# Optimization experiments

Measured on AMD Instinct MI355X. Metric: run time of the kernel, lower is better.

The kernel has to match this reference:

```python
import jax, jax.numpy as jnp
import numpy as np

B, L, C = 64, 64, 16          # batch, seq_len, chars per word
V, CV = 100000, 100           # word vocab, char vocab
EMB, CHD = 300, 64            # word emb dim, char emb dim
N_HIGHWAY, N_ATTN = 2, 2
D = EMB + 3 * 50              # highway_dim = 450


def setup_inputs() -> dict:
    ks = jax.random.split(jax.random.key(0), 16)
    word_emb = jax.random.normal(ks[6], (V, EMB), jnp.float32) * 0.01
    word_emb = word_emb.at[0].set(0.0)  # padding_idx row zeroed
    return {
        "q1": jax.random.randint(ks[0], (B, L), 0, V),
        "q2": jax.random.randint(ks[1], (B, L), 0, V),
        "q1_len": jax.random.randint(ks[2], (B,), 1, L + 1),
        "q2_len": jax.random.randint(ks[3], (B,), 1, L + 1),
        "q1_char": jax.random.randint(ks[4], (B, L, C), 0, CV),
        "q2_char": jax.random.randint(ks[5], (B, L, C), 0, CV),
        "word_emb": word_emb,
        "char_emb": jax.random.normal(ks[7], (CV, CHD), jnp.float32) * 0.1,
        "conv_w3": jax.random.normal(ks[8], (50, CHD, 3), jnp.float32) / np.sqrt(CHD * 3),
        "conv_b3": jnp.zeros((50,), jnp.float32),
        "conv_w4": jax.random.normal(ks[9], (50, CHD, 4), jnp.float32) / np.sqrt(CHD * 4),
        "conv_b4": jnp.zeros((50,), jnp.float32),
        "conv_w5": jax.random.normal(ks[10], (50, CHD, 5), jnp.float32) / np.sqrt(CHD * 5),
        "conv_b5": jnp.zeros((50,), jnp.float32),
        "hw_w": jax.random.normal(ks[11], (D, D), jnp.float32) / np.sqrt(D),
        "hw_b": jnp.zeros((D,), jnp.float32),
        "attn_w": jax.random.normal(ks[12], (N_ATTN, 3 * D), jnp.float32) / np.sqrt(3 * D),
        "attn_b": jnp.zeros((N_ATTN,), jnp.float32),
    }


def _char_features(qc, emb, convs):
    # qc: [B, T, C] int -> [B, T, 150]
    Bq, T, Cc = qc.shape
    e = emb[qc.reshape(-1, Cc)].transpose(0, 2, 1)  # [B*T, CHD, C]
    outs = []
    for w, b in convs:
        h = jax.lax.conv_general_dilated(e, w, (1,), 'VALID',
                                         dimension_numbers=('NCH', 'OIH', 'NCH'))
        h = jax.nn.relu(h + b[None, :, None])
        outs.append(jnp.max(h, axis=2))  # max over char positions
    return jnp.concatenate(outs, axis=-1).reshape(Bq, T, -1)


def _highway(x, w, b):
    # NB: original reuses the SAME linear for transform and gate (bug-faithful)
    y = x @ w.T + b
    g = jax.nn.sigmoid(y)
    return g * jax.nn.relu(y) + (1.0 - g) * x


def _self_attn(x, mask, w, b):
    # Exact decomposition of Linear(concat(x_i, x_j, x_i*x_j)) -> scalar:
    # score[b,i,j] = x_i.w1 + x_j.w2 + sum_d x_i x_j w3 + b
    d = x.shape[-1]
    w1, w2, w3 = w[:d], w[d:2 * d], w[2 * d:]
    scores = ((x @ w1)[:, :, None] + (x @ w2)[:, None, :]
              + jnp.einsum('bid,bjd->bij', x * w3, x) + b)
    # original masked_fill uses -1e-09 (not -1e9) -- reproduce faithfully
    logits = jnp.where(mask[:, None, :], scores, jnp.float32(-1e-9))
    attn = jax.nn.softmax(logits, axis=-1)
    return jnp.einsum('bij,bjd->bid', attn, x)


def _branch(q, q_char, q_len, word_emb, char_emb, convs, hw_w, hw_b, attn_w, attn_b):
    mask = jnp.arange(L)[None, :] < q_len[:, None]
    x = jnp.concatenate([word_emb[q], _char_features(q_char, char_emb, convs)], axis=-1)
    for _ in range(N_HIGHWAY):
        x = _highway(x, hw_w, hw_b)
    att = x
    for i in range(N_ATTN):
        att = _self_attn(x, mask, attn_w[i], attn_b[i])
        x = att + x
    return att


def reference(q1, q2, q1_len, q2_len, q1_char, q2_char, word_emb, char_emb,
              conv_w3, conv_b3, conv_w4, conv_b4, conv_w5, conv_b5,
              hw_w, hw_b, attn_w, attn_b):
    convs = [(conv_w3, conv_b3), (conv_w4, conv_b4), (conv_w5, conv_b5)]
    a1 = _branch(q1, q1_char, q1_len, word_emb, char_emb, convs, hw_w, hw_b, attn_w, attn_b)
    a2 = _branch(q2, q2_char, q2_len, word_emb, char_emb, convs, hw_w, hw_b, attn_w, attn_b)
    return (a1, a2)
```

## Files before the change

kernel.cpp:

```cpp
#include <hip/hip_runtime.h>
#include <math.h>

#define B   64
#define L   64
#define C   16
#define CHD 64
#define EMB 300
#define D   450
#define DP  480
#define NT  (B*L)
#define NBH 128

typedef short bf16x8 __attribute__((ext_vector_type(8)));
typedef float f32x4  __attribute__((ext_vector_type(4)));
typedef float f32x2  __attribute__((ext_vector_type(2)));
typedef unsigned short ushort_t;
typedef ushort_t us4 __attribute__((ext_vector_type(4)));

#define MFMA16 __builtin_amdgcn_mfma_f32_16x16x32_bf16

#define WPF_N (10 * 10 * 512)
#define WBF_N (32 * 15 * 512)
#define XFRAG 30720

__device__ inline float wave_sum(float v) {
#pragma unroll
    for (int o = 32; o; o >>= 1) v += __shfl_xor(v, o, 64);
    return v;
}
__device__ inline ushort_t f2b(float f) {
    union { float f; unsigned u; } c; c.f = f;
    unsigned r = c.u + 0x7FFFu + ((c.u >> 16) & 1u);
    return (ushort_t)(r >> 16);
}

__global__ __launch_bounds__(256) void prep_kernel(
    const float* __restrict__ W,
    const float* __restrict__ w3, const float* __restrict__ b3,
    const float* __restrict__ w4, const float* __restrict__ b4,
    const float* __restrict__ w5, const float* __restrict__ b5,
    const float* __restrict__ char_emb,
    ushort_t* __restrict__ Wb16F, ushort_t* __restrict__ WpadF,
    float* __restrict__ bias160, ushort_t* __restrict__ ceb16)
{
    int idx = blockIdx.x * 256 + threadIdx.x;
    if (idx < WBF_N) {
        const int e = idx & 7, l = (idx >> 3) & 63, t = idx >> 9;
        const int ks = t % 15, nt = t / 15;
        const int ln = l & 15, q = l >> 4;
        const int n = nt * 16 + ln, k = ks * 32 + q * 8 + e;
        float v = (n < D && k < D) ? W[(size_t)n * D + k] : 0.f;
        Wb16F[idx] = f2b(v);
        return;
    }
    idx -= WBF_N;
    if (idx < WPF_N) {
        const int e = idx & 7, l = (idx >> 3) & 63, t = idx >> 9;
        const int ks = t % 10, nt = t / 10;
        const int ln = l & 15, q = l >> 4;
        const int f = nt * 16 + ln;
        const int kd = ks * 32 + q * 8 + e;
        const int k = kd >> 6, d = kd & 63;
        float v = 0.f;
        if (f < 50)       { if (k < 3) v = w3[f * 192 + d * 3 + k]; }
        else if (f < 100) { if (k < 4) v = w4[(f - 50) * 256 + d * 4 + k]; }
        else if (f < 150) { v = w5[(f - 100) * 320 + d * 5 + k]; }
        WpadF[idx] = f2b(v);
        return;
    }
    idx -= WPF_N;
    if (idx < 160) {
        bias160[idx] = (idx < 50) ? b3[idx] : (idx < 100) ? b4[idx - 50]
                     : (idx < 150) ? b5[idx - 100] : 0.f;
    } else if (idx < 160 + 100 * 64) {
        int i = idx - 160;
        ceb16[i] = f2b(char_emb[i]);
    }
}

#define ESS 72
#define EST (20 * ESS)

__global__ __launch_bounds__(256) void embed_conv_kernel(
    const int* __restrict__ q1, const int* __restrict__ q2,
    const int* __restrict__ q1c, const int* __restrict__ q2c,
    const float* __restrict__ word_emb, const ushort_t* __restrict__ ceb16,
    const ushort_t* __restrict__ WpadF, const float* __restrict__ bias160,
    float* __restrict__ xout, ushort_t* __restrict__ xb16)
{
    __shared__ ushort_t es[8 * EST];

    const int tid  = threadIdx.x;
    const int wv   = tid >> 6;
    const int lane = tid & 63;
    const int ln   = lane & 15, quad = lane >> 4;
    const int bx   = blockIdx.x;
    const int tokbase = ((bx & 7) * 128 + (bx >> 3)) * 8;

#pragma unroll
    for (int i = 0; i < 4; ++i) {
        int c = tid + i * 256;
        int row = c >> 3, part = c & 7;
        int tl = row >> 4, cr = row & 15;
        int gtok   = tokbase + tl;
        int branch = gtok >> 12;
        int tokl   = gtok & (NT - 1);
        int cid    = (branch ? q2c : q1c)[tokl * C + cr];
        *(bf16x8*)&es[tl * EST + cr * ESS + part * 8] =
            *(const bf16x8*)&ceb16[cid * 64 + part * 8];
    }
    {
        int tl = tid >> 5, rr = (tid >> 3) & 3, part = tid & 7;
        bf16x8 z = {0, 0, 0, 0, 0, 0, 0, 0};
        *(bf16x8*)&es[tl * EST + (16 + rr) * ESS + part * 8] = z;
    }

#pragma unroll 1
    for (int c = tid; c < 8 * 75; c += 256) {
        const int t  = c / 75, d4 = c - t * 75;
        const int tok    = tokbase + t;
        const int branch = tok >> 12;
        const int tokl   = tok & (NT - 1);
        const int w      = (branch ? q2 : q1)[tokl];
        const float4 v = *(const float4*)(word_emb + (size_t)w * EMB + d4 * 4);
        float* dst = xout + (size_t)tok * D + d4 * 4;
        *(f32x2*)dst       = (f32x2){v.x, v.y};
        *(f32x2*)(dst + 2) = (f32x2){v.z, v.w};
        us4 pk = { f2b(v.x), f2b(v.y), f2b(v.z), f2b(v.w) };
        *(us4*)(xb16 + (size_t)tok * DP + d4 * 4) = pk;
    }
    if (tid < 240) {
        const int t = tid / 30, k = tid - t * 30;
        xb16[(size_t)(tokbase + t) * DP + D + k] = 0;
    }
    __syncthreads();

    const int t0 = wv * 2, t1 = t0 + 1;
    f32x4 acc[2][10];
#pragma unroll
    for (int t = 0; t < 2; ++t)
#pragma unroll
        for (int nt = 0; nt < 10; ++nt) acc[t][nt] = (f32x4){0.f, 0.f, 0.f, 0.f};

#pragma unroll 1
    for (int ks = 0; ks < 10; ++ks) {
        const int kk   = ks * 32 + quad * 8;
        const int arow = kk >> 6, aoff = kk & 63;
        bf16x8 a0 = *(const bf16x8*)&es[t0 * EST + (ln + arow) * ESS + aoff];
        bf16x8 a1 = *(const bf16x8*)&es[t1 * EST + (ln + arow) * ESS + aoff];
#pragma unroll
        for (int nt = 0; nt < 10; ++nt) {
            bf16x8 bf = *(const bf16x8*)&WpadF[(size_t)((nt * 10 + ks) << 9) + lane * 8];
            acc[0][nt] = MFMA16(a0, bf, acc[0][nt], 0, 0, 0);
            acc[1][nt] = MFMA16(a1, bf, acc[1][nt], 0, 0, 0);
        }
    }
    __syncthreads();

    float* smf = (float*)es;
#pragma unroll
    for (int t = 0; t < 2; ++t) {
        const int tloc = t0 + t;
#pragma unroll
        for (int nt = 0; nt < 10; ++nt) {
            const int f  = nt * 16 + ln;
            const int Pf = (f < 50) ? 14 : (f < 100) ? 13 : 12;
            float m = -1e30f;
#pragma unroll
            for (int r = 0; r < 4; ++r) {
                const int p = quad * 4 + r;
                if (p < Pf) m = fmaxf(m, acc[t][nt][r]);
            }
            m = fmaxf(m, __shfl_xor(m, 16, 64));
            m = fmaxf(m, __shfl_xor(m, 32, 64));
            if (quad == 0) smf[tloc * 160 + f] = fmaxf(0.f, m + bias160[f]);
        }
    }
    __syncthreads();
#pragma unroll 1
    for (int c = tid; c < 8 * 150; c += 256) {
        const int t = c / 150, f = c - t * 150;
        const float rv = smf[t * 160 + f];
        xout[(size_t)(tokbase + t) * D + EMB + f] = rv;
        xb16[(size_t)(tokbase + t) * DP + EMB + f] = f2b(rv);
    }
}

__global__ __launch_bounds__(256, 4) void highway_mfma_kernel(
    const ushort_t* __restrict__ xb16, const float* __restrict__ xf32,
    const ushort_t* __restrict__ Wb16F, const float* __restrict__ bvec,
    float* __restrict__ out, ushort_t* __restrict__ outb16)
{
    const int bx = blockIdx.x;
    const int cx = bx & 7, rr = bx >> 3;
    const int my = cx * 16 + (rr & 15);
    const int mx = rr >> 4;

    const int tid  = threadIdx.x;
    const int wv   = tid >> 6;
    const int lane = tid & 63;
    const int wm = wv >> 1, wn = wv & 1;
    const int m0 = my * 64 + wm * 32;
    const int n0 = mx * 64 + wn * 32;
    const int lm = lane & 15, quad = lane >> 4;

    const ushort_t* ax  = xb16 + (size_t)(m0 + lm) * DP + quad * 8;
    const int ntg0 = mx * 4 + wn * 2;
    const ushort_t* bw0 = Wb16F + (size_t)(ntg0 * 15) * 512 + lane * 8;
    const ushort_t* bw1 = bw0 + 15 * 512;

    f32x4 acc[2][2];
#pragma unroll
    for (int i = 0; i < 2; ++i)
#pragma unroll
        for (int j = 0; j < 2; ++j) acc[i][j] = (f32x4){0.f, 0.f, 0.f, 0.f};

#pragma unroll 3
    for (int ks = 0; ks < 15; ++ks) {
        bf16x8 a0 = *(const bf16x8*)(ax + ks * 32);
        bf16x8 a1 = *(const bf16x8*)(ax + (size_t)16 * DP + ks * 32);
        bf16x8 b0 = *(const bf16x8*)(bw0 + ks * 512);
        bf16x8 b1 = *(const bf16x8*)(bw1 + ks * 512);
        acc[0][0] = MFMA16(a0, b0, acc[0][0], 0, 0, 0);
        acc[0][1] = MFMA16(a0, b1, acc[0][1], 0, 0, 0);
        acc[1][0] = MFMA16(a1, b0, acc[1][0], 0, 0, 0);
        acc[1][1] = MFMA16(a1, b1, acc[1][1], 0, 0, 0);
    }

#pragma unroll
    for (int nt = 0; nt < 2; ++nt) {
        const int n = n0 + nt * 16 + lm;
        const bool nval = (n < D);
        const float bv = nval ? bvec[n] : 0.f;
#pragma unroll
        for (int mt = 0; mt < 2; ++mt) {
#pragma unroll
            for (int r = 0; r < 4; ++r) {
                const int m = m0 + mt * 16 + quad * 4 + r;
                float y = acc[mt][nt][r] + bv;
                float g = 1.f / (1.f + __expf(-y));
                float o = 0.f;
                if (nval) {
                    float xo = xf32[(size_t)m * D + n];
                    o = g * fmaxf(y, 0.f) + (1.f - g) * xo;
                    out[(size_t)m * D + n] = o;
                }
                if (n < DP)
                    outb16[(size_t)m * DP + n] = f2b(nval ? o : 0.f);
            }
        }
    }
}

#define PXS 496

__global__ __launch_bounds__(256) void attn_prep_kernel(
    const float* __restrict__ xf32, const float* __restrict__ attn_w, int layer,
    ushort_t* __restrict__ xF, ushort_t* __restrict__ xw3F, ushort_t* __restrict__ xTF,
    float* __restrict__ s1g, float* __restrict__ s2g)
{
    __shared__ ushort_t Xs[16 * PXS];
    __shared__ ushort_t Xw3s[16 * PXS];

    const int bx  = blockIdx.x;
    const int wid = (bx & 7) * 64 + (bx >> 3);
    const int bh  = wid >> 2, jq = wid & 3;
    const int tid = threadIdx.x;
    const int wv  = tid >> 6;
    const int lane = tid & 63;
    const size_t tok0 = (size_t)bh * 64 + jq * 16;

    const float* wb = attn_w + (size_t)layer * 3 * D;
    const float* w3 = wb + 2 * D;

#pragma unroll 1
    for (int c = tid; c < 16 * 60; c += 256) {
        const int j  = c / 60, k8 = c - j * 60;
        const int k0 = k8 * 8;
        const float* xr = xf32 + (tok0 + j) * D;
        bf16x8 xv, pv;
#pragma unroll
        for (int t = 0; t < 8; ++t) {
            const int k = k0 + t;
            const float x = (k < D) ? xr[k] : 0.f;
            xv[t] = (short)f2b(x);
            pv[t] = (short)f2b((k < D) ? x * w3[k] : 0.f);
        }
        *(bf16x8*)&Xs[j * PXS + k0]   = xv;
        *(bf16x8*)&Xw3s[j * PXS + k0] = pv;
    }

#pragma unroll 1
    for (int rr = 0; rr < 4; ++rr) {
        const int j = wv * 4 + rr;
        const float* xr = xf32 + (tok0 + j) * D;
        float a1 = 0.f, a2 = 0.f;
#pragma unroll
        for (int t = 0; t < 8; ++t) {
            const int k = lane + t * 64;
            if (k < D) {
                float xv = xr[k];
                a1 = fmaf(xv, wb[k], a1);
                a2 = fmaf(xv, wb[D + k], a2);
            }
        }
        a1 = wave_sum(a1);
        a2 = wave_sum(a2);
        if (lane == 0) { s1g[tok0 + j] = a1; s2g[tok0 + j] = a2; }
    }
    __syncthreads();

#pragma unroll 1
    for (int c = tid; c < 960; c += 256) {
        const int ks = c >> 6, l = c & 63;
        const int lnp = l & 15, qp = l >> 4;
        bf16x8 v = *(const bf16x8*)&Xs[lnp * PXS + ks * 32 + qp * 8];
        bf16x8 w = *(const bf16x8*)&Xw3s[lnp * PXS + ks * 32 + qp * 8];
        const size_t o = (size_t)bh * XFRAG + ((jq * 15 + ks) * 64 + l) * 8;
        *(bf16x8*)&xF[o]   = v;
        *(bf16x8*)&xw3F[o] = w;
    }

    {
        const int half = jq >> 1, q0 = (jq & 1) * 2;
#pragma unroll 1
        for (int c = tid; c < 960; c += 256) {
            const int dt = c >> 5, s = c & 31;
            const int qp = q0 + (s >> 4), lnp = s & 15;
            const int d  = dt * 16 + lnp;
            const int jb = (qp & 1) * 8;
            bf16x8 v;
#pragma unroll
            for (int e = 0; e < 8; ++e) v[e] = (short)Xs[(jb + e) * PXS + d];
            *(bf16x8*)&xTF[(size_t)bh * XFRAG + ((dt * 2 + half) * 64 + qp * 16 + lnp) * 8] = v;
        }
    }
}

#define ALS 72

template <bool RES_EMIT>
__global__ __launch_bounds__(256) void attn_fused_kernel(
    const float* __restrict__ xf32,
    const ushort_t* __restrict__ xF, const ushort_t* __restrict__ xw3F,
    const ushort_t* __restrict__ xTF,
    const float* __restrict__ s1g, const float* __restrict__ s2g,
    const int* __restrict__ q1_len, const int* __restrict__ q2_len,
    const float* __restrict__ attn_b, int layer,
    float* __restrict__ outf)
{
    __shared__ float    sc[16][68];
    __shared__ ushort_t Al[16 * ALS];

    const int bx  = blockIdx.x;
    const int wid = (bx & 7) * 64 + (bx >> 3);
    const int bh  = wid >> 2, iq = wid & 3;
    const int branch = bh >> 6, b = bh & 63;
    const int tid  = threadIdx.x;
    const int wv   = tid >> 6;
    const int lane = tid & 63;
    const int ln   = lane & 15, quad = lane >> 4;
    const int i0   = iq * 16;

    const ushort_t* xa = xF   + (size_t)bh * XFRAG + (iq * 15 * 64 + lane) * 8;
    const ushort_t* xb = xw3F + (size_t)bh * XFRAG + (wv * 15 * 64 + lane) * 8;

    f32x4 qa0 = (f32x4){0.f, 0.f, 0.f, 0.f};
    f32x4 qa1 = (f32x4){0.f, 0.f, 0.f, 0.f};
#pragma unroll
    for (int ks = 0; ks < 14; ks += 2) {
        bf16x8 a0 = *(const bf16x8*)(xa + ks * 512);
        bf16x8 b0 = *(const bf16x8*)(xb + ks * 512);
        bf16x8 a1 = *(const bf16x8*)(xa + ks * 512 + 512);
        bf16x8 b1 = *(const bf16x8*)(xb + ks * 512 + 512);
        qa0 = MFMA16(a0, b0, qa0, 0, 0, 0);
        qa1 = MFMA16(a1, b1, qa1, 0, 0, 0);
    }
    {
        bf16x8 a  = *(const bf16x8*)(xa + 14 * 512);
        bf16x8 bq = *(const bf16x8*)(xb + 14 * 512);
        qa0 = MFMA16(a, bq, qa0, 0, 0, 0);
    }
    f32x4 qacc = qa0 + qa1;

    const int   len  = (branch ? q2_len : q1_len)[b];
    const float bias = attn_b[layer];
    const int   j    = wv * 16 + ln;
    const float s2v  = s2g[bh * 64 + j];
#pragma unroll
    for (int reg = 0; reg < 4; ++reg) {
        const int i = i0 + quad * 4 + reg;
        float v = qacc[reg] + s1g[bh * 64 + i] + s2v + bias;
        if (j >= len) v = -1e-9f;
        sc[quad * 4 + reg][j] = v;
    }
    __syncthreads();

#pragma unroll
    for (int rr = 0; rr < 4; ++rr) {
        const int r = wv * 4 + rr;
        float v = sc[r][lane];
        float m = v;
#pragma unroll
        for (int o = 32; o; o >>= 1) m = fmaxf(m, __shfl_xor(m, o, 64));
        float ev = __expf(v - m);
        float sm = ev;
#pragma unroll
        for (int o = 32; o; o >>= 1) sm += __shfl_xor(sm, o, 64);
        Al[r * ALS + lane] = f2b(ev * (1.f / sm));
    }
    __syncthreads();

    const ushort_t* xTb = xTF + (size_t)bh * XFRAG + lane * 8;
    bf16x8 af0 = *(const bf16x8*)&Al[ln * ALS + quad * 8];
    bf16x8 af1 = *(const bf16x8*)&Al[ln * ALS + quad * 8 + 32];

#pragma unroll 2
    for (int dt = wv; dt < 30; dt += 4) {
        bf16x8 b0 = *(const bf16x8*)(xTb + dt * 1024);
        bf16x8 b1 = *(const bf16x8*)(xTb + dt * 1024 + 512);
        f32x4 acc = (f32x4){0.f, 0.f, 0.f, 0.f};
        acc = MFMA16(af0, b0, acc, 0, 0, 0);
        acc = MFMA16(af1, b1, acc, 0, 0, 0);

        const int d = dt * 16 + ln;
        if (d < D) {
#pragma unroll
            for (int reg = 0; reg < 4; ++reg) {
                const int i = i0 + quad * 4 + reg;
                float v = acc[reg];
                if (RES_EMIT) v += xf32[((size_t)bh * 64 + i) * D + d];
                outf[((size_t)bh * 64 + i) * D + d] = v;
            }
        }
    }
}

extern "C" void kernel_launch(void* const* d_in, const int* in_sizes, int n_in,
                              void* d_out, int out_size, void* d_ws, size_t ws_size,
                              hipStream_t stream) {
    const int*   q1       = (const int*)  d_in[0];
    const int*   q2       = (const int*)  d_in[1];
    const int*   q1_len   = (const int*)  d_in[2];
    const int*   q2_len   = (const int*)  d_in[3];
    const int*   q1c      = (const int*)  d_in[4];
    const int*   q2c      = (const int*)  d_in[5];
    const float* word_emb = (const float*)d_in[6];
    const float* char_emb = (const float*)d_in[7];
    const float* w3       = (const float*)d_in[8];
    const float* b3       = (const float*)d_in[9];
    const float* w4       = (const float*)d_in[10];
    const float* b4       = (const float*)d_in[11];
    const float* w5       = (const float*)d_in[12];
    const float* b5       = (const float*)d_in[13];
    const float* hw_w     = (const float*)d_in[14];
    const float* hw_b     = (const float*)d_in[15];
    const float* attn_w   = (const float*)d_in[16];
    const float* attn_b   = (const float*)d_in[17];
    float* out = (float*)d_out;

    float*    buf0    = (float*)d_ws;
    float*    buf1    = buf0 + (size_t)2 * NT * D;
    float*    bias160 = buf1 + (size_t)2 * NT * D;
    ushort_t* xb16a   = (ushort_t*)(bias160 + 160);
    ushort_t* xb16b   = xb16a + (size_t)2 * NT * DP;
    ushort_t* Wb16F   = xb16b + (size_t)2 * NT * DP;
    ushort_t* WpadF   = Wb16F + (size_t)WBF_N;
    ushort_t* ceb16   = WpadF + (size_t)WPF_N;
    ushort_t* xF      = ceb16 + (size_t)100 * 64;
    ushort_t* xw3F    = xF   + (size_t)NBH * XFRAG;
    ushort_t* xTF     = xw3F + (size_t)NBH * XFRAG;
    float*    s1g     = (float*)(xTF + (size_t)NBH * XFRAG);
    float*    s2g     = s1g + (size_t)2 * NT;

    prep_kernel<<<(WBF_N + WPF_N + 160 + 100 * 64 + 255) / 256, 256, 0, stream>>>(
        hw_w, w3, b3, w4, b4, w5, b5, char_emb, Wb16F, WpadF, bias160, ceb16);
    embed_conv_kernel<<<1024, 256, 0, stream>>>(q1, q2, q1c, q2c, word_emb, ceb16,
                                                WpadF, bias160, buf0, xb16a);

    highway_mfma_kernel<<<1024, 256, 0, stream>>>(xb16a, buf0, Wb16F, hw_b, buf1, xb16b);
    highway_mfma_kernel<<<1024, 256, 0, stream>>>(xb16b, buf1, Wb16F, hw_b, buf0, xb16a);

    attn_prep_kernel<<<512, 256, 0, stream>>>(buf0, attn_w, 0, xF, xw3F, xTF, s1g, s2g);
    attn_fused_kernel<true><<<512, 256, 0, stream>>>(
        buf0, xF, xw3F, xTF, s1g, s2g, q1_len, q2_len, attn_b, 0, buf1);

    attn_prep_kernel<<<512, 256, 0, stream>>>(buf1, attn_w, 1, xF, xw3F, xTF, s1g, s2g);
    attn_fused_kernel<false><<<512, 256, 0, stream>>>(
        buf1, xF, xw3F, xTF, s1g, s2g, q1_len, q2_len, attn_b, 1, out);
}
```

Before: 339.8 us.

## Store bf16 activations in MFMA fragment layout across kernels, drop xF rewrite

The producers (embed_conv, highway, first attention layer) now stage their bf16 activation outputs in shared memory and write them in the pre-swizzled MFMA fragment layout. Highway then loads A operands as contiguous per-lane 16-byte chunks, and the attention kernels read the same buffer directly. This lets attn_prep skip building and writing its separate xF fragment copy. In exchange each producer gets extra LDS, a barrier and a transpose pass, and the highway kernel's shared-memory use may reduce occupancy.

```diff
diff --git a/kernel.cpp b/kernel.cpp
--- a/kernel.cpp
+++ b/kernel.cpp
@@ -80,15 +80,17 @@
 
 #define ESS 72
 #define EST (20 * ESS)
+#define XTS1 488
 
 __global__ __launch_bounds__(256) void embed_conv_kernel(
     const int* __restrict__ q1, const int* __restrict__ q2,
     const int* __restrict__ q1c, const int* __restrict__ q2c,
     const float* __restrict__ word_emb, const ushort_t* __restrict__ ceb16,
     const ushort_t* __restrict__ WpadF, const float* __restrict__ bias160,
-    float* __restrict__ xout, ushort_t* __restrict__ xb16)
+    float* __restrict__ xout, ushort_t* __restrict__ xbF)
 {
     __shared__ ushort_t es[8 * EST];
+    __shared__ ushort_t Xt[8 * XTS1];
 
     const int tid  = threadIdx.x;
     const int wv   = tid >> 6;
@@ -127,11 +129,11 @@
         *(f32x2*)dst       = (f32x2){v.x, v.y};
         *(f32x2*)(dst + 2) = (f32x2){v.z, v.w};
         us4 pk = { f2b(v.x), f2b(v.y), f2b(v.z), f2b(v.w) };
-        *(us4*)(xb16 + (size_t)tok * DP + d4 * 4) = pk;
+        *(us4*)&Xt[t * XTS1 + d4 * 4] = pk;
     }
     if (tid < 240) {
         const int t = tid / 30, k = tid - t * 30;
-        xb16[(size_t)(tokbase + t) * DP + D + k] = 0;
+        Xt[t * XTS1 + D + k] = 0;
     }
     __syncthreads();
 
@@ -182,15 +184,32 @@
         const int t = c / 150, f = c - t * 150;
         const float rv = smf[t * 160 + f];
         xout[(size_t)(tokbase + t) * D + EMB + f] = rv;
-        xb16[(size_t)(tokbase + t) * DP + EMB + f] = f2b(rv);
-    }
-}
+        Xt[t * XTS1 + EMB + f] = f2b(rv);
+    }
+    __syncthreads();
+
+    {
+        const int tile = tokbase >> 4, half = (tokbase >> 3) & 1;
+#pragma unroll 1
+        for (int c = tid; c < 480; c += 256) {
+            const int ksl = c >> 5, s = c & 31;
+            const int q = s >> 3, tl = s & 7;
+            const int l = q * 16 + half * 8 + tl;
+            bf16x8 v = *(const bf16x8*)&Xt[tl * XTS1 + ksl * 32 + q * 8];
+            *(bf16x8*)&xbF[((size_t)(tile * 15 + ksl) * 64 + l) * 8] = v;
+        }
+    }
+}
+
+#define HLS 72
 
 __global__ __launch_bounds__(256, 4) void highway_mfma_kernel(
-    const ushort_t* __restrict__ xb16, const float* __restrict__ xf32,
+    const ushort_t* __restrict__ xbFi, const float* __restrict__ xf32,
     const ushort_t* __restrict__ Wb16F, const float* __restrict__ bvec,
-    float* __restrict__ out, ushort_t* __restrict__ outb16)
+    float* __restrict__ out, ushort_t* __restrict__ xbFo)
 {
+    __shared__ ushort_t Xl[64 * HLS];
+
     const int bx = blockIdx.x;
     const int cx = bx & 7, rr = bx >> 3;
     const int my = cx * 16 + (rr & 15);
@@ -204,7 +223,9 @@
     const int n0 = mx * 64 + wn * 32;
     const int lm = lane & 15, quad = lane >> 4;
 
-    const ushort_t* ax  = xb16 + (size_t)(m0 + lm) * DP + quad * 8;
+    const int tA0 = my * 4 + wm * 2;
+    const ushort_t* ax0 = xbFi + (size_t)(tA0 * 15) * 512 + lane * 8;
+    const ushort_t* ax1 = ax0 + 15 * 512;
     const int ntg0 = mx * 4 + wn * 2;
     const ushort_t* bw0 = Wb16F + (size_t)(ntg0 * 15) * 512 + lane * 8;
     const ushort_t* bw1 = bw0 + 15 * 512;
@@ -217,8 +238,8 @@
 
 #pragma unroll 3
     for (int ks = 0; ks < 15; ++ks) {
-        bf16x8 a0 = *(const bf16x8*)(ax + ks * 32);
-        bf16x8 a1 = *(const bf16x8*)(ax + (size_t)16 * DP + ks * 32);
+        bf16x8 a0 = *(const bf16x8*)(ax0 + ks * 512);
+        bf16x8 a1 = *(const bf16x8*)(ax1 + ks * 512);
         bf16x8 b0 = *(const bf16x8*)(bw0 + ks * 512);
         bf16x8 b1 = *(const bf16x8*)(bw1 + ks * 512);
         acc[0][0] = MFMA16(a0, b0, acc[0][0], 0, 0, 0);
@@ -229,14 +250,16 @@
 
 #pragma unroll
     for (int nt = 0; nt < 2; ++nt) {
-        const int n = n0 + nt * 16 + lm;
+        const int n  = n0 + nt * 16 + lm;
+        const int nl = wn * 32 + nt * 16 + lm;
         const bool nval = (n < D);
         const float bv = nval ? bvec[n] : 0.f;
 #pragma unroll
         for (int mt = 0; mt < 2; ++mt) {
 #pragma unroll
             for (int r = 0; r < 4; ++r) {
-                const int m = m0 + mt * 16 + quad * 4 + r;
+                const int m  = m0 + mt * 16 + quad * 4 + r;
+                const int ml = wm * 32 + mt * 16 + quad * 4 + r;
                 float y = acc[mt][nt][r] + bv;
                 float g = 1.f / (1.f + __expf(-y));
                 float o = 0.f;
@@ -245,9 +268,21 @@
                     o = g * fmaxf(y, 0.f) + (1.f - g) * xo;
                     out[(size_t)m * D + n] = o;
                 }
-                if (n < DP)
-                    outb16[(size_t)m * DP + n] = f2b(nval ? o : 0.f);
+                Xl[ml * HLS + nl] = f2b(nval ? o : 0.f);
             }
+        }
+    }
+    __syncthreads();
+
+#pragma unroll 1
+    for (int c = tid; c < 512; c += 256) {
+        const int fi = c >> 6, l = c & 63;
+        const int tl = fi >> 1, ksl = fi & 1;
+        const int ksg = mx * 2 + ksl;
+        if (ksg < 15) {
+            const int lnp = l & 15, qp = l >> 4;
+            bf16x8 v = *(const bf16x8*)&Xl[(tl * 16 + lnp) * HLS + ksl * 32 + qp * 8];
+            *(bf16x8*)&xbFo[((size_t)((my * 4 + tl) * 15 + ksg) * 64 + l) * 8] = v;
         }
     }
 }
@@ -256,7 +291,7 @@
 
 __global__ __launch_bounds__(256) void attn_prep_kernel(
     const float* __restrict__ xf32, const float* __restrict__ attn_w, int layer,
-    ushort_t* __restrict__ xF, ushort_t* __restrict__ xw3F, ushort_t* __restrict__ xTF,
+    ushort_t* __restrict__ xw3F, ushort_t* __restrict__ xTF,
     float* __restrict__ s1g, float* __restrict__ s2g)
 {
     __shared__ ushort_t Xs[16 * PXS];
@@ -314,11 +349,8 @@
     for (int c = tid; c < 960; c += 256) {
         const int ks = c >> 6, l = c & 63;
         const int lnp = l & 15, qp = l >> 4;
-        bf16x8 v = *(const bf16x8*)&Xs[lnp * PXS + ks * 32 + qp * 8];
         bf16x8 w = *(const bf16x8*)&Xw3s[lnp * PXS + ks * 32 + qp * 8];
-        const size_t o = (size_t)bh * XFRAG + ((jq * 15 + ks) * 64 + l) * 8;
-        *(bf16x8*)&xF[o]   = v;
-        *(bf16x8*)&xw3F[o] = w;
+        *(bf16x8*)&xw3F[(size_t)bh * XFRAG + ((jq * 15 + ks) * 64 + l) * 8] = w;
     }
 
     {
@@ -347,10 +379,11 @@
     const float* __restrict__ s1g, const float* __restrict__ s2g,
     const int* __restrict__ q1_len, const int* __restrict__ q2_len,
     const float* __restrict__ attn_b, int layer,
-    float* __restrict__ outf)
+    float* __restrict__ outf, ushort_t* __restrict__ xbFo)
 {
     __shared__ float    sc[16][68];
     __shared__ ushort_t Al[16 * ALS];
+    __shared__ ushort_t At[RES_EMIT ? 16 * XTS1 : 8];
 
     const int bx  = blockIdx.x;
     const int wid = (bx & 7) * 64 + (bx >> 3);
@@ -362,6 +395,13 @@
     const int ln   = lane & 15, quad = lane >> 4;
     const int i0   = iq * 16;
 
+    if (RES_EMIT) {
+        for (int c = tid; c < 480; c += 256) {
+            const int t = c / 30, k = c - t * 30;
+            At[t * XTS1 + D + k] = 0;
+        }
+    }
+
     const ushort_t* xa = xF   + (size_t)bh * XFRAG + (iq * 15 * 64 + lane) * 8;
     const ushort_t* xb = xw3F + (size_t)bh * XFRAG + (wv * 15 * 64 + lane) * 8;
 
@@ -431,7 +471,20 @@
                 float v = acc[reg];
                 if (RES_EMIT) v += xf32[((size_t)bh * 64 + i) * D + d];
                 outf[((size_t)bh * 64 + i) * D + d] = v;
+                if (RES_EMIT)
+                    At[(quad * 4 + reg) * XTS1 + d] = f2b(v);
             }
+        }
+    }
+
+    if (RES_EMIT) {
+        __syncthreads();
+#pragma unroll 1
+        for (int c = tid; c < 960; c += 256) {
+            const int ksl = c >> 6, l = c & 63;
+            const int lnp = l & 15, qp = l >> 4;
+            bf16x8 v = *(const bf16x8*)&At[lnp * XTS1 + ksl * 32 + qp * 8];
+            *(bf16x8*)&xbFo[((size_t)((bh * 4 + iq) * 15 + ksl) * 64 + l) * 8] = v;
         }
     }
 }
@@ -462,13 +515,12 @@
     float*    buf0    = (float*)d_ws;
     float*    buf1    = buf0 + (size_t)2 * NT * D;
     float*    bias160 = buf1 + (size_t)2 * NT * D;
-    ushort_t* xb16a   = (ushort_t*)(bias160 + 160);
-    ushort_t* xb16b   = xb16a + (size_t)2 * NT * DP;
-    ushort_t* Wb16F   = xb16b + (size_t)2 * NT * DP;
+    ushort_t* xbFa    = (ushort_t*)(bias160 + 160);
+    ushort_t* xbFb    = xbFa + (size_t)2 * NT * DP;
+    ushort_t* Wb16F   = xbFb + (size_t)2 * NT * DP;
     ushort_t* WpadF   = Wb16F + (size_t)WBF_N;
     ushort_t* ceb16   = WpadF + (size_t)WPF_N;
-    ushort_t* xF      = ceb16 + (size_t)100 * 64;
-    ushort_t* xw3F    = xF   + (size_t)NBH * XFRAG;
+    ushort_t* xw3F    = ceb16 + (size_t)100 * 64;
     ushort_t* xTF     = xw3F + (size_t)NBH * XFRAG;
     float*    s1g     = (float*)(xTF + (size_t)NBH * XFRAG);
     float*    s2g     = s1g + (size_t)2 * NT;
@@ -476,16 +528,16 @@
     prep_kernel<<<(WBF_N + WPF_N + 160 + 100 * 64 + 255) / 256, 256, 0, stream>>>(
         hw_w, w3, b3, w4, b4, w5, b5, char_emb, Wb16F, WpadF, bias160, ceb16);
     embed_conv_kernel<<<1024, 256, 0, stream>>>(q1, q2, q1c, q2c, word_emb, ceb16,
-                                                WpadF, bias160, buf0, xb16a);
-
-    highway_mfma_kernel<<<1024, 256, 0, stream>>>(xb16a, buf0, Wb16F, hw_b, buf1, xb16b);
-    highway_mfma_kernel<<<1024, 256, 0, stream>>>(xb16b, buf1, Wb16F, hw_b, buf0, xb16a);
-
-    attn_prep_kernel<<<512, 256, 0, stream>>>(buf0, attn_w, 0, xF, xw3F, xTF, s1g, s2g);
+                                                WpadF, bias160, buf0, xbFa);
+
+    highway_mfma_kernel<<<1024, 256, 0, stream>>>(xbFa, buf0, Wb16F, hw_b, buf1, xbFb);
+    highway_mfma_kernel<<<1024, 256, 0, stream>>>(xbFb, buf1, Wb16F, hw_b, buf0, xbFa);
+
+    attn_prep_kernel<<<512, 256, 0, stream>>>(buf0, attn_w, 0, xw3F, xTF, s1g, s2g);
     attn_fused_kernel<true><<<512, 256, 0, stream>>>(
-        buf0, xF, xw3F, xTF, s1g, s2g, q1_len, q2_len, attn_b, 0, buf1);
-
-    attn_prep_kernel<<<512, 256, 0, stream>>>(buf1, attn_w, 1, xF, xw3F, xTF, s1g, s2g);
+        buf0, xbFa, xw3F, xTF, s1g, s2g, q1_len, q2_len, attn_b, 0, buf1, xbFb);
+
+    attn_prep_kernel<<<512, 256, 0, stream>>>(buf1, attn_w, 1, xw3F, xTF, s1g, s2g);
     attn_fused_kernel<false><<<512, 256, 0, stream>>>(
-        buf1, xF, xw3F, xTF, s1g, s2g, q1_len, q2_len, attn_b, 1, out);
-}
+        buf1, xbFb, xw3F, xTF, s1g, s2g, q1_len, q2_len, attn_b, 1, out, nullptr);
+}
```

Measured after the change: 323.3 us. -4.8%, faster.
